# Kernel tuning notes

Hardware: AMD Instinct MI355X
Metric: run time of the kernel (lower is better)

Reference implementation:

```python
import jax, jax.numpy as jnp
import numpy as np

B, T, D, H = 4, 2048, 1024, 16
HD = D // H  # head_dim = 64


def setup_inputs() -> dict:
    key = jax.random.key(0)
    ks = jax.random.split(key, 7)
    x = jax.random.normal(ks[0], (B, T, D), dtype=jnp.float32)
    engagement = jax.random.uniform(ks[1], (B, T), dtype=jnp.float32)
    mask = jax.random.uniform(ks[2], (B, T)) < 0.1  # True = masked-out key
    s = 1.0 / np.sqrt(D)
    qkv_w = jax.random.normal(ks[3], (3 * D, D), dtype=jnp.float32) * s
    qkv_b = jax.random.normal(ks[4], (3 * D,), dtype=jnp.float32) * 0.02
    out_w = jax.random.normal(ks[5], (D, D), dtype=jnp.float32) * s
    out_b = jax.random.normal(ks[6], (D,), dtype=jnp.float32) * 0.02
    return {"x": x, "engagement": engagement, "mask": mask,
            "qkv_w": qkv_w, "qkv_b": qkv_b, "out_w": out_w, "out_b": out_b}


def reference(x, engagement, mask, qkv_w, qkv_b, out_w, out_b):
    b, t, d = x.shape
    qkv = x @ qkv_w.T + qkv_b                       # [B,T,3D]
    q, k, v = jnp.split(qkv, 3, axis=-1)
    # [B,T,D] -> [B,H,T,HD]
    to_heads = lambda a: a.reshape(b, t, H, HD).transpose(0, 2, 1, 3)
    q, k, v = to_heads(q), to_heads(k), to_heads(v)
    attn = jnp.einsum('bhqd,bhkd->bhqk', q, k) / jnp.sqrt(jnp.float32(HD))
    log_g = jnp.log(jnp.clip(engagement, 1e-6))     # [B,T] per-key bias
    attn = attn + log_g[:, None, None, :]
    attn = jnp.where(mask[:, None, None, :], jnp.float32(-1e9), attn)
    p = jax.nn.softmax(attn, axis=-1)
    o = jnp.einsum('bhqk,bhkd->bhqd', p, v)         # [B,H,T,HD]
    o = o.transpose(0, 2, 1, 3).reshape(b, t, d)    # [B,T,D]
    return o @ out_w.T + out_b
```

## Files before the change

kernel.cpp:

```cpp
#include <hip/hip_runtime.h>
#include <math.h>

#define B_  4
#define T_  2048
#define D_  1024
#define H_  16
#define HD_ 64

typedef unsigned short ushort_t;
typedef unsigned int uint_t;
typedef __attribute__((ext_vector_type(8))) short bf16x8;
typedef __attribute__((ext_vector_type(4))) float f32x4;

#define SC_LOG2 0.1803368801111243f

__device__ inline ushort_t f2bf(float f) {
  uint_t u = __float_as_uint(f);
  u += 0x7fffu + ((u >> 16) & 1u);
  return (ushort_t)(u >> 16);
}
__device__ inline ushort_t f2bf_fast(float f) {
  return (ushort_t)((__float_as_uint(f) + 0x8000u) >> 16);
}
__device__ inline uint_t cvtpk_bf16(float lo, float hi) {
  uint_t r;
  asm("v_cvt_pk_bf16_f32 %0, %1, %2" : "=v"(r) : "v"(lo), "v"(hi));
  return r;
}

__device__ inline void gload_lds16(const ushort_t* g, ushort_t* l) {
  __builtin_amdgcn_global_load_lds(
      (const __attribute__((address_space(1))) unsigned int*)g,
      (__attribute__((address_space(3))) unsigned int*)l, 16, 0, 0);
}

__global__ __launch_bounds__(256) void cvt_bf16(const float* __restrict__ in,
                                                ushort_t* __restrict__ out, int n) {
  int i = (blockIdx.x * 256 + threadIdx.x) * 4;
  if (i + 3 < n) {
    float4 v = *(const float4*)(in + i);
    uint_t lo = (uint_t)f2bf(v.x) | ((uint_t)f2bf(v.y) << 16);
    uint_t hi = (uint_t)f2bf(v.z) | ((uint_t)f2bf(v.w) << 16);
    *(uint2*)(out + i) = make_uint2(lo, hi);
  }
}

__global__ __launch_bounds__(256) void bias_prep(const float* __restrict__ eng,
                                                 const int* __restrict__ mask,
                                                 float* __restrict__ biasA, int n) {
  int i = blockIdx.x * 256 + threadIdx.x;
  if (i < n) biasA[i] = mask[i] ? -1e30f : __log2f(fmaxf(eng[i], 1e-6f));
}

#define CHUNKS_ 32

#define STAGE_CHUNK(CK, SLOT)                                                  \
  {                                                                            \
    const int ck_ = (CK);                                                      \
    ushort_t* la_ = lds + (SLOT) * 16384 + wA * 32;                            \
    _Pragma("unroll")                                                          \
    for (int u = 0; u < 2; ++u) {                                              \
      gload_lds16(Ag + (size_t)u * 16384 + ck_ * 32, la_ + u * 512);           \
      gload_lds16(Bg + (size_t)u * 16384 + ck_ * 32, la_ + 8192 + u * 512);    \
    }                                                                          \
  }

template <int WRITE_BF16>
__global__ __launch_bounds__(512, 2) void gemm256(
    const ushort_t* __restrict__ A, const ushort_t* __restrict__ Bm,
    const float* __restrict__ bias, void* __restrict__ Cout,
    int N, int nbx) {
  __shared__ __align__(16) ushort_t lds[65536];

  const int tid = threadIdx.x;
  const int w = tid >> 6, lane = tid & 63;
  const int l15 = lane & 15, quad = lane >> 4;
  const int wr = w >> 2, wc = w & 3;

  int wg = blockIdx.x;
  const int cpx = gridDim.x >> 3;
  wg = (wg & 7) * cpx + (wg >> 3);
  const int m0 = (wg / nbx) * 256, n0 = (wg % nbx) * 256;

  const int gc = (lane & 3) ^ ((lane >> 3) & 3);
  const ushort_t* Ag = A + (size_t)(m0 + w * 32 + (lane >> 2)) * 1024 + gc * 8;
  const ushort_t* Bg = Bm + (size_t)(n0 + w * 32 + (lane >> 2)) * 1024 + gc * 8;
  const int wA = w * 32;

  const int p8 = (quad ^ ((l15 >> 1) & 3)) * 8;
  const int rowA = (wr * 128 + l15) * 32 + p8;
  const int rowB = 8192 + (wc * 64 + l15) * 32 + p8;

  f32x4 acc[8][4];
#pragma unroll
  for (int mb = 0; mb < 8; ++mb)
#pragma unroll
    for (int nb = 0; nb < 4; ++nb) acc[mb][nb] = (f32x4){0.f, 0.f, 0.f, 0.f};

  STAGE_CHUNK(0, 0);
  STAGE_CHUNK(1, 1);
  STAGE_CHUNK(2, 2);
  asm volatile("s_waitcnt vmcnt(8)" ::: "memory");
  __builtin_amdgcn_s_barrier();
  __builtin_amdgcn_sched_barrier(0);

#pragma unroll 1
  for (int ph = 0; ph < CHUNKS_; ++ph) {
    const ushort_t* Ls = lds + (ph & 3) * 16384;
    bf16x8 af[8], bf[4];
#pragma unroll
    for (int mb = 0; mb < 8; ++mb)
      af[mb] = *(const bf16x8*)(Ls + rowA + mb * 512);
#pragma unroll
    for (int nb = 0; nb < 4; ++nb)
      bf[nb] = *(const bf16x8*)(Ls + rowB + nb * 512);
    if (ph < CHUNKS_ - 3) {
      STAGE_CHUNK(ph + 3, (ph + 3) & 3);
    }
    __builtin_amdgcn_s_setprio(1);
#pragma unroll
    for (int mb = 0; mb < 8; ++mb)
#pragma unroll
      for (int nb = 0; nb < 4; ++nb)
        acc[mb][nb] = __builtin_amdgcn_mfma_f32_16x16x32_bf16(
            af[mb], bf[nb], acc[mb][nb], 0, 0, 0);
    __builtin_amdgcn_s_setprio(0);
    if (ph < CHUNKS_ - 3)
      asm volatile("s_waitcnt vmcnt(8)" ::: "memory");
    else if (ph == CHUNKS_ - 3)
      asm volatile("s_waitcnt vmcnt(4)" ::: "memory");
    else
      asm volatile("s_waitcnt vmcnt(0)" ::: "memory");
    __builtin_amdgcn_s_barrier();
    __builtin_amdgcn_sched_barrier(0);
  }

  float bb[4];
#pragma unroll
  for (int nb = 0; nb < 4; ++nb) bb[nb] = bias[n0 + wc * 64 + nb * 16 + l15];

  if (WRITE_BF16) {
    ushort_t* patch = lds + w * 5120;
    ushort_t* Cb = (ushort_t*)Cout;
#pragma unroll
    for (int half = 0; half < 2; ++half) {
#pragma unroll
      for (int mb4 = 0; mb4 < 4; ++mb4) {
#pragma unroll
        for (int nb = 0; nb < 4; ++nb)
#pragma unroll
          for (int i = 0; i < 4; ++i)
            patch[(mb4 * 16 + quad * 4 + i) * 80 + nb * 16 + l15] =
                f2bf_fast(acc[half * 4 + mb4][nb][i] + bb[nb]);
      }
#pragma unroll
      for (int it = 0; it < 8; ++it) {
        int rl = it * 8 + (lane >> 3);
        size_t grow = (size_t)(m0 + wr * 128 + half * 64 + rl);
        uint4 v = *(const uint4*)&patch[rl * 80 + (lane & 7) * 8];
        *(uint4*)&Cb[grow * N + n0 + wc * 64 + (lane & 7) * 8] = v;
      }
    }
  } else {
    float* Cf = (float*)Cout;
#pragma unroll
    for (int mb = 0; mb < 8; ++mb)
#pragma unroll
      for (int i = 0; i < 4; ++i) {
        size_t row = (size_t)(m0 + wr * 128 + mb * 16 + quad * 4 + i);
#pragma unroll
        for (int nb = 0; nb < 4; ++nb)
          Cf[row * N + n0 + wc * 64 + nb * 16 + l15] = acc[mb][nb][i] + bb[nb];
      }
  }
}

#define ATTN_TILE(K0, Kc, Vc, bc, Kn, Vn, bn, PF)                              \
  {                                                                            \
    uint4 va_, vc_;                                                            \
    const bool pf_ = (PF);                                                     \
    if (pf_) {                                                                 \
      const int k1_ = (K0) + 64;                                               \
      _Pragma("unroll")                                                        \
      for (int u = 0; u < 2; ++u)                                              \
        gload_lds16(kbase + (size_t)(k1_ + w * 16 + u * 8 + kr) * rs + kgc * 8,\
                    &(Kn)[(w * 16 + u * 8) * 64]);                             \
      const ushort_t* vp_ = vbase + (size_t)(k1_ + 2 * kp) * rs + cc * 8;      \
      va_ = *(const uint4*)vp_;                                                \
      vc_ = *(const uint4*)(vp_ + rs);                                         \
      if (tid < 64) (bn)[tid] = bptr[k1_ + tid];                               \
    }                                                                          \
    bf16x8 kf0[4], kf1[4];                                                     \
    _Pragma("unroll")                                                          \
    for (int nb = 0; nb < 4; ++nb) {                                           \
      int key = nb * 16 + l15;                                                 \
      int p0 = (quad ^ (key & 7)) * 8;                                         \
      kf0[nb] = *(const bf16x8*)(&(Kc)[key * 64 + p0]);                        \
      kf1[nb] = *(const bf16x8*)(&(Kc)[key * 64 + (p0 ^ 32)]);                 \
    }                                                                          \
    bf16x8 vf0[4], vf1[4];                                                     \
    _Pragma("unroll")                                                          \
    for (int nbd = 0; nbd < 4; ++nbd) {                                        \
      vf0[nbd] = *(const bf16x8*)(&(Vc)[quad * 520 + (nbd * 16 + l15) * 8]);   \
      vf1[nbd] =                                                               \
          *(const bf16x8*)(&(Vc)[(4 + quad) * 520 + (nbd * 16 + l15) * 8]);    \
    }                                                                          \
    _Pragma("unroll")                                                          \
    for (int qb = 0; qb < 2; ++qb) {                                           \
      f32x4 st[4];                                                             \
      __builtin_amdgcn_s_setprio(1);                                           \
      _Pragma("unroll")                                                        \
      for (int nb = 0; nb < 4; ++nb) {                                         \
        f32x4 s = (f32x4){0.f, 0.f, 0.f, 0.f};                                 \
        s = __builtin_amdgcn_mfma_f32_16x16x32_bf16(kf0[nb], qf[qb][0], s, 0,  \
                                                    0, 0);                     \
        s = __builtin_amdgcn_mfma_f32_16x16x32_bf16(kf1[nb], qf[qb][1], s, 0,  \
                                                    0, 0);                     \
        st[nb] = s;                                                            \
      }                                                                        \
      __builtin_amdgcn_s_setprio(0);                                           \
      float pp[4][4];                                                          \
      float racc = 0.f;                                                        \
      _Pragma("unroll")                                                        \
      for (int nb = 0; nb < 4; ++nb) {                                         \
        f32x4 bv = *(const f32x4*)&(bc)[nb * 16 + quad * 4];                   \
        _Pragma("unroll")                                                      \
        for (int i = 0; i < 4; ++i) {                                          \
          float p = __builtin_amdgcn_exp2f(st[nb][i] * SC_LOG2 + bv[i]);       \
          pp[nb][i] = p;                                                       \
          racc += p;                                                           \
        }                                                                      \
      }                                                                        \
      rsum[qb] += racc;                                                        \
      union { uint4 u; bf16x8 v; } pf0, pf1;                                   \
      pf0.u.x = cvtpk_bf16(pp[0][0], pp[0][1]);                                \
      pf0.u.y = cvtpk_bf16(pp[0][2], pp[0][3]);                                \
      pf0.u.z = cvtpk_bf16(pp[1][0], pp[1][1]);                                \
      pf0.u.w = cvtpk_bf16(pp[1][2], pp[1][3]);                                \
      pf1.u.x = cvtpk_bf16(pp[2][0], pp[2][1]);                                \
      pf1.u.y = cvtpk_bf16(pp[2][2], pp[2][3]);                                \
      pf1.u.z = cvtpk_bf16(pp[3][0], pp[3][1]);                                \
      pf1.u.w = cvtpk_bf16(pp[3][2], pp[3][3]);                                \
      __builtin_amdgcn_s_setprio(1);                                           \
      _Pragma("unroll")                                                        \
      for (int nbd = 0; nbd < 4; ++nbd) {                                      \
        Oa[qb][nbd] = __builtin_amdgcn_mfma_f32_16x16x32_bf16(                 \
            pf0.v, vf0[nbd], Oa[qb][nbd], 0, 0, 0);                            \
        Oa[qb][nbd] = __builtin_amdgcn_mfma_f32_16x16x32_bf16(                 \
            pf1.v, vf1[nbd], Oa[qb][nbd], 0, 0, 0);                            \
      }                                                                        \
      __builtin_amdgcn_s_setprio(0);                                           \
    }                                                                          \
    if (pf_) {                                                                 \
      uint_t* dst_ = (uint_t*)&(Vn)[gp * 520 + cc * 64 + j0];                  \
      dst_[0]  = (va_.x & 0xffffu) | (vc_.x << 16);                            \
      dst_[4]  = (va_.x >> 16)     | (vc_.x & 0xffff0000u);                    \
      dst_[8]  = (va_.y & 0xffffu) | (vc_.y << 16);                            \
      dst_[12] = (va_.y >> 16)     | (vc_.y & 0xffff0000u);                    \
      dst_[16] = (va_.z & 0xffffu) | (vc_.z << 16);                            \
      dst_[20] = (va_.z >> 16)     | (vc_.z & 0xffff0000u);                    \
      dst_[24] = (va_.w & 0xffffu) | (vc_.w << 16);                            \
      dst_[28] = (va_.w >> 16)     | (vc_.w & 0xffff0000u);                    \
    }                                                                          \
    __syncthreads();                                                           \
  }

__global__ __launch_bounds__(256) void attn_mfma(
    const ushort_t* __restrict__ qkv, const float* __restrict__ biasA,
    ushort_t* __restrict__ oat) {
  __shared__ __align__(16) char smem[34048];
  ushort_t* Kb0 = (ushort_t*)(smem);
  ushort_t* Kb1 = (ushort_t*)(smem + 8192);
  ushort_t* Vb0 = (ushort_t*)(smem + 16384);
  ushort_t* Vb1 = (ushort_t*)(smem + 24704);
  float* bsh0 = (float*)(smem + 33024);
  float* bsh1 = (float*)(smem + 33280);
  float (*lsum)[32] = (float (*)[32])(smem + 33536);

  const int b = blockIdx.z, h = blockIdx.y;
  const int q0 = blockIdx.x * 128;
  const int tid = threadIdx.x;
  const int w = tid >> 6, lane = tid & 63;
  const int l15 = lane & 15, quad = lane >> 4;
  const size_t rs = 3 * D_;

  bf16x8 qf[2][2];
#pragma unroll
  for (int qb = 0; qb < 2; ++qb) {
    const ushort_t* qp =
        qkv + (size_t)(b * T_ + q0 + w * 32 + qb * 16 + l15) * rs + h * HD_;
    qf[qb][0] = *(const bf16x8*)(qp + quad * 8);
    qf[qb][1] = *(const bf16x8*)(qp + 32 + quad * 8);
  }

  f32x4 Oa[2][4];
#pragma unroll
  for (int qb = 0; qb < 2; ++qb)
#pragma unroll
    for (int nb = 0; nb < 4; ++nb) Oa[qb][nb] = (f32x4){0.f, 0.f, 0.f, 0.f};
  float rsum[2] = {0.f, 0.f};

  const ushort_t* kbase = qkv + (size_t)(b * T_) * rs + D_ + h * HD_;
  const ushort_t* vbase = kbase + D_;
  const float* bptr = biasA + b * T_;

  const int kr = lane >> 3, kc = lane & 7;
  const int kgc = kc ^ kr;
  const int kp = tid & 31, cc = tid >> 5;
  const int gp = (kp >> 4) * 4 + ((kp >> 1) & 3);
  const int j0 = ((kp >> 3) & 1) * 4 + 2 * (kp & 1);

  {
#pragma unroll
    for (int u = 0; u < 2; ++u)
      gload_lds16(kbase + (size_t)(w * 16 + u * 8 + kr) * rs + kgc * 8,
                  &Kb0[(w * 16 + u * 8) * 64]);
    const ushort_t* vp = vbase + (size_t)(2 * kp) * rs + cc * 8;
    uint4 va = *(const uint4*)vp;
    uint4 vc = *(const uint4*)(vp + rs);
    if (tid < 64) bsh0[tid] = bptr[tid];
    uint_t* dst = (uint_t*)&Vb0[gp * 520 + cc * 64 + j0];
    dst[0]  = (va.x & 0xffffu) | (vc.x << 16);
    dst[4]  = (va.x >> 16)     | (vc.x & 0xffff0000u);
    dst[8]  = (va.y & 0xffffu) | (vc.y << 16);
    dst[12] = (va.y >> 16)     | (vc.y & 0xffff0000u);
    dst[16] = (va.z & 0xffffu) | (vc.z << 16);
    dst[20] = (va.z >> 16)     | (vc.z & 0xffff0000u);
    dst[24] = (va.w & 0xffffu) | (vc.w << 16);
    dst[28] = (va.w >> 16)     | (vc.w & 0xffff0000u);
  }
  __syncthreads();

  for (int k0 = 0; k0 < T_; k0 += 128) {
    ATTN_TILE(k0,      Kb0, Vb0, bsh0, Kb1, Vb1, bsh1, true);
    ATTN_TILE(k0 + 64, Kb1, Vb1, bsh1, Kb0, Vb0, bsh0, k0 + 128 < T_);
  }

#pragma unroll
  for (int qb = 0; qb < 2; ++qb) {
    float r = rsum[qb];
    r += __shfl_xor(r, 16, 64);
    r += __shfl_xor(r, 32, 64);
    if (lane < 16) lsum[w][qb * 16 + lane] = r;
  }
  ushort_t* OstW = (ushort_t*)(smem) + w * (32 * 72);
#pragma unroll
  for (int qb = 0; qb < 2; ++qb) {
    f32x4 lr = *(const f32x4*)&lsum[w][qb * 16 + quad * 4];
    f32x4 invl;
#pragma unroll
    for (int i = 0; i < 4; ++i) invl[i] = __builtin_amdgcn_rcpf(lr[i]);
#pragma unroll
    for (int nbd = 0; nbd < 4; ++nbd)
#pragma unroll
      for (int i = 0; i < 4; ++i)
        OstW[(qb * 16 + quad * 4 + i) * 72 + nbd * 16 + l15] =
            f2bf_fast(Oa[qb][nbd][i] * invl[i]);
  }
  ushort_t* dst = oat + (size_t)(b * T_ + q0 + w * 32) * D_ + h * HD_;
#pragma unroll
  for (int pp = 0; pp < 4; ++pp) {
    int row = pp * 8 + (lane >> 3), c = lane & 7;
    uint4 v = *(const uint4*)&OstW[row * 72 + c * 8];
    *(uint4*)&dst[(size_t)row * D_ + c * 8] = v;
  }
}

extern "C" void kernel_launch(void* const* d_in, const int* in_sizes, int n_in,
                              void* d_out, int out_size, void* d_ws, size_t ws_size,
                              hipStream_t stream) {
  const float* x     = (const float*)d_in[0];
  const float* eng   = (const float*)d_in[1];
  const int*   mask  = (const int*)d_in[2];
  const float* qkv_w = (const float*)d_in[3];
  const float* qkv_b = (const float*)d_in[4];
  const float* out_w = (const float*)d_in[5];
  const float* out_b = (const float*)d_in[6];
  float* out = (float*)d_out;

  const int M = B_ * T_;
  const size_t nx = (size_t)M * D_;
  const size_t nwq = (size_t)3 * D_ * D_;
  const size_t nwo = (size_t)D_ * D_;
  const size_t nqkv = (size_t)M * 3 * D_;

  char* p = (char*)d_ws;
  ushort_t* xb    = (ushort_t*)p;            p += nx * 2;
  ushort_t* wqkvb = (ushort_t*)p;            p += nwq * 2;
  ushort_t* woutb = (ushort_t*)p;            p += nwo * 2;
  ushort_t* qkvb  = (ushort_t*)p;            p += nqkv * 2;
  ushort_t* oatb  = (ushort_t*)p;            p += nx * 2;
  float*    biasA = (float*)p;               p += (size_t)M * 4;

  cvt_bf16<<<(int)(nx / 1024), 256, 0, stream>>>(x, xb, (int)nx);
  cvt_bf16<<<(int)(nwq / 1024), 256, 0, stream>>>(qkv_w, wqkvb, (int)nwq);
  cvt_bf16<<<(int)(nwo / 1024), 256, 0, stream>>>(out_w, woutb, (int)nwo);
  bias_prep<<<M / 256, 256, 0, stream>>>(eng, mask, biasA, M);

  gemm256<1><<<384, 512, 0, stream>>>(xb, wqkvb, qkv_b, qkvb, 3 * D_, 12);
  attn_mfma<<<dim3(T_ / 128, H_, B_), 256, 0, stream>>>(qkvb, biasA, oatb);
  gemm256<0><<<128, 512, 0, stream>>>(oatb, woutb, out_b, out, D_, 4);
}
```

Before: 320.5 us.

## Halve GEMM M-tile to 128 with 3-stage LDS pipeline and doubled grid

```diff
diff --git a/kernel.cpp b/kernel.cpp
--- a/kernel.cpp
+++ b/kernel.cpp
@@ -57,20 +57,18 @@
 #define STAGE_CHUNK(CK, SLOT)                                                  \
   {                                                                            \
     const int ck_ = (CK);                                                      \
-    ushort_t* la_ = lds + (SLOT) * 16384 + wA * 32;                            \
-    _Pragma("unroll")                                                          \
-    for (int u = 0; u < 2; ++u) {                                              \
-      gload_lds16(Ag + (size_t)u * 16384 + ck_ * 32, la_ + u * 512);           \
-      gload_lds16(Bg + (size_t)u * 16384 + ck_ * 32, la_ + 8192 + u * 512);    \
-    }                                                                          \
+    ushort_t* sb_ = lds + (SLOT) * 12288;                                      \
+    gload_lds16(Ag + (size_t)ck_ * 32, sb_ + w * 512);                         \
+    gload_lds16(Bg + (size_t)ck_ * 32, sb_ + 4096 + w * 1024);                 \
+    gload_lds16(Bg + 16384 + (size_t)ck_ * 32, sb_ + 4096 + w * 1024 + 512);   \
   }
 
 template <int WRITE_BF16>
-__global__ __launch_bounds__(512, 2) void gemm256(
+__global__ __launch_bounds__(512, 4) void gemm256(
     const ushort_t* __restrict__ A, const ushort_t* __restrict__ Bm,
     const float* __restrict__ bias, void* __restrict__ Cout,
     int N, int nbx) {
-  __shared__ __align__(16) ushort_t lds[65536];
+  __shared__ __align__(16) ushort_t lds[36864];
 
   const int tid = threadIdx.x;
   const int w = tid >> 6, lane = tid & 63;
@@ -80,59 +78,58 @@
   int wg = blockIdx.x;
   const int cpx = gridDim.x >> 3;
   wg = (wg & 7) * cpx + (wg >> 3);
-  const int m0 = (wg / nbx) * 256, n0 = (wg % nbx) * 256;
+  const int m0 = (wg / nbx) * 128, n0 = (wg % nbx) * 256;
 
   const int gc = (lane & 3) ^ ((lane >> 3) & 3);
-  const ushort_t* Ag = A + (size_t)(m0 + w * 32 + (lane >> 2)) * 1024 + gc * 8;
+  const ushort_t* Ag = A + (size_t)(m0 + w * 16 + (lane >> 2)) * 1024 + gc * 8;
   const ushort_t* Bg = Bm + (size_t)(n0 + w * 32 + (lane >> 2)) * 1024 + gc * 8;
-  const int wA = w * 32;
 
   const int p8 = (quad ^ ((l15 >> 1) & 3)) * 8;
-  const int rowA = (wr * 128 + l15) * 32 + p8;
-  const int rowB = 8192 + (wc * 64 + l15) * 32 + p8;
-
-  f32x4 acc[8][4];
-#pragma unroll
-  for (int mb = 0; mb < 8; ++mb)
+  const int rowA = (wr * 64 + l15) * 32 + p8;
+  const int rowB = 4096 + (wc * 64 + l15) * 32 + p8;
+
+  f32x4 acc[4][4];
+#pragma unroll
+  for (int mb = 0; mb < 4; ++mb)
 #pragma unroll
     for (int nb = 0; nb < 4; ++nb) acc[mb][nb] = (f32x4){0.f, 0.f, 0.f, 0.f};
 
   STAGE_CHUNK(0, 0);
   STAGE_CHUNK(1, 1);
-  STAGE_CHUNK(2, 2);
-  asm volatile("s_waitcnt vmcnt(8)" ::: "memory");
+  asm volatile("s_waitcnt vmcnt(3)" ::: "memory");
   __builtin_amdgcn_s_barrier();
   __builtin_amdgcn_sched_barrier(0);
 
+  int s_cur = 0;
 #pragma unroll 1
   for (int ph = 0; ph < CHUNKS_; ++ph) {
-    const ushort_t* Ls = lds + (ph & 3) * 16384;
-    bf16x8 af[8], bf[4];
-#pragma unroll
-    for (int mb = 0; mb < 8; ++mb)
+    const ushort_t* Ls = lds + s_cur * 12288;
+    bf16x8 af[4], bf[4];
+#pragma unroll
+    for (int mb = 0; mb < 4; ++mb)
       af[mb] = *(const bf16x8*)(Ls + rowA + mb * 512);
 #pragma unroll
     for (int nb = 0; nb < 4; ++nb)
       bf[nb] = *(const bf16x8*)(Ls + rowB + nb * 512);
-    if (ph < CHUNKS_ - 3) {
-      STAGE_CHUNK(ph + 3, (ph + 3) & 3);
+    if (ph < CHUNKS_ - 2) {
+      const int s_n2 = (s_cur == 0) ? 2 : s_cur - 1;
+      STAGE_CHUNK(ph + 2, s_n2);
     }
     __builtin_amdgcn_s_setprio(1);
 #pragma unroll
-    for (int mb = 0; mb < 8; ++mb)
+    for (int mb = 0; mb < 4; ++mb)
 #pragma unroll
       for (int nb = 0; nb < 4; ++nb)
         acc[mb][nb] = __builtin_amdgcn_mfma_f32_16x16x32_bf16(
             af[mb], bf[nb], acc[mb][nb], 0, 0, 0);
     __builtin_amdgcn_s_setprio(0);
-    if (ph < CHUNKS_ - 3)
-      asm volatile("s_waitcnt vmcnt(8)" ::: "memory");
-    else if (ph == CHUNKS_ - 3)
-      asm volatile("s_waitcnt vmcnt(4)" ::: "memory");
+    if (ph < CHUNKS_ - 2)
+      asm volatile("s_waitcnt vmcnt(3)" ::: "memory");
     else
       asm volatile("s_waitcnt vmcnt(0)" ::: "memory");
     __builtin_amdgcn_s_barrier();
     __builtin_amdgcn_sched_barrier(0);
+    s_cur = (s_cur == 2) ? 0 : s_cur + 1;
   }
 
   float bb[4];
@@ -140,34 +137,30 @@
   for (int nb = 0; nb < 4; ++nb) bb[nb] = bias[n0 + wc * 64 + nb * 16 + l15];
 
   if (WRITE_BF16) {
-    ushort_t* patch = lds + w * 5120;
+    ushort_t* patch = lds + w * 4608;
     ushort_t* Cb = (ushort_t*)Cout;
 #pragma unroll
-    for (int half = 0; half < 2; ++half) {
-#pragma unroll
-      for (int mb4 = 0; mb4 < 4; ++mb4) {
-#pragma unroll
-        for (int nb = 0; nb < 4; ++nb)
-#pragma unroll
-          for (int i = 0; i < 4; ++i)
-            patch[(mb4 * 16 + quad * 4 + i) * 80 + nb * 16 + l15] =
-                f2bf_fast(acc[half * 4 + mb4][nb][i] + bb[nb]);
-      }
-#pragma unroll
-      for (int it = 0; it < 8; ++it) {
-        int rl = it * 8 + (lane >> 3);
-        size_t grow = (size_t)(m0 + wr * 128 + half * 64 + rl);
-        uint4 v = *(const uint4*)&patch[rl * 80 + (lane & 7) * 8];
-        *(uint4*)&Cb[grow * N + n0 + wc * 64 + (lane & 7) * 8] = v;
-      }
+    for (int mb = 0; mb < 4; ++mb)
+#pragma unroll
+      for (int nb = 0; nb < 4; ++nb)
+#pragma unroll
+        for (int i = 0; i < 4; ++i)
+          patch[(mb * 16 + quad * 4 + i) * 72 + nb * 16 + l15] =
+              f2bf_fast(acc[mb][nb][i] + bb[nb]);
+#pragma unroll
+    for (int it = 0; it < 8; ++it) {
+      int rl = it * 8 + (lane >> 3);
+      size_t grow = (size_t)(m0 + wr * 64 + rl);
+      uint4 v = *(const uint4*)&patch[rl * 72 + (lane & 7) * 8];
+      *(uint4*)&Cb[grow * N + n0 + wc * 64 + (lane & 7) * 8] = v;
     }
   } else {
     float* Cf = (float*)Cout;
 #pragma unroll
-    for (int mb = 0; mb < 8; ++mb)
+    for (int mb = 0; mb < 4; ++mb)
 #pragma unroll
       for (int i = 0; i < 4; ++i) {
-        size_t row = (size_t)(m0 + wr * 128 + mb * 16 + quad * 4 + i);
+        size_t row = (size_t)(m0 + wr * 64 + mb * 16 + quad * 4 + i);
 #pragma unroll
         for (int nb = 0; nb < 4; ++nb)
           Cf[row * N + n0 + wc * 64 + nb * 16 + l15] = acc[mb][nb][i] + bb[nb];
@@ -397,7 +390,7 @@
   cvt_bf16<<<(int)(nwo / 1024), 256, 0, stream>>>(out_w, woutb, (int)nwo);
   bias_prep<<<M / 256, 256, 0, stream>>>(eng, mask, biasA, M);
 
-  gemm256<1><<<384, 512, 0, stream>>>(xb, wqkvb, qkv_b, qkvb, 3 * D_, 12);
+  gemm256<1><<<768, 512, 0, stream>>>(xb, wqkvb, qkv_b, qkvb, 3 * D_, 12);
   attn_mfma<<<dim3(T_ / 128, H_, B_), 256, 0, stream>>>(qkvb, biasA, oatb);
-  gemm256<0><<<128, 512, 0, stream>>>(oatb, woutb, out_b, out, D_, 4);
-}
+  gemm256<0><<<256, 512, 0, stream>>>(oatb, woutb, out_b, out, D_, 4);
+}
```

New measurement: 295.9 us. 1.08x faster.
